# Optimization experiments

Measured on AMD Instinct MI355X. Metric: run time of the kernel, lower is better.

## Reference

```python
import jax, jax.numpy as jnp
import numpy as np
from jax import lax

NUM_HEADS = 8


def setup_inputs() -> dict:
    key = jax.random.key(0)
    ks = jax.random.split(key, 6)
    B, L, Hd = 4, 4096, 512
    S = 45  # factor * ceil(ln(L)) = 5 * 9
    x = jax.random.normal(ks[0], (B, L, Hd), dtype=jnp.float32)
    scale = 1.0 / np.sqrt(Hd)
    Wq = jax.random.normal(ks[1], (Hd, Hd), dtype=jnp.float32) * scale
    Wk = jax.random.normal(ks[2], (Hd, Hd), dtype=jnp.float32) * scale
    Wv = jax.random.normal(ks[3], (Hd, Hd), dtype=jnp.float32) * scale
    Wo = jax.random.normal(ks[4], (Hd, Hd), dtype=jnp.float32) * scale
    index_sample = jax.random.randint(ks[5], (L, S), 0, L, dtype=jnp.int32)
    return {"x": x, "Wq": Wq, "Wk": Wk, "Wv": Wv, "Wo": Wo,
            "index_sample": index_sample}


def reference(x, Wq, Wk, Wv, Wo, index_sample):
    B, L, Hd = x.shape
    H = NUM_HEADS
    D = Hd // H
    S = index_sample.shape[1]
    u = S  # n_top active queries = factor*ceil(ln(L))

    def split_heads(t):  # [B,L,Hd] -> [B,H,L,D]
        return t.reshape(B, L, H, D).transpose(0, 2, 1, 3)

    q = split_heads(x @ Wq)
    k = split_heads(x @ Wk)
    v = split_heads(x @ Wv)

    scale = 1.0 / jnp.sqrt(jnp.asarray(D, dtype=x.dtype))

    # sampled key gather: [B,H,L,S,D]
    K_samp = k[:, :, index_sample, :]
    # sampled scores per query: [B,H,L,S]
    QK_samp = jnp.einsum('bhld,bhlsd->bhls', q, K_samp)
    # sparsity measurement: max - mean over sampled keys
    M = QK_samp.max(axis=-1) - QK_samp.mean(axis=-1)  # [B,H,L]
    _, top_idx = lax.top_k(M, u)                      # [B,H,u]

    # full attention only for active queries
    Qr = jnp.take_along_axis(q, top_idx[..., None], axis=2)   # [B,H,u,D]
    scores = jnp.einsum('bhud,bhld->bhul', Qr, k) * scale     # [B,H,u,L]
    attn = jax.nn.softmax(scores, axis=-1)
    ctx_sel = jnp.einsum('bhul,bhld->bhud', attn, v)          # [B,H,u,D]

    # inactive queries get mean(V); scatter active results in
    context = jnp.broadcast_to(v.mean(axis=2, keepdims=True), (B, H, L, D))
    b_idx = jnp.arange(B)[:, None, None]
    h_idx = jnp.arange(H)[None, :, None]
    context = context.at[b_idx, h_idx, top_idx].set(ctx_sel)

    out = context.transpose(0, 2, 1, 3).reshape(B, L, Hd) @ Wo
    return out
```

## Files before the change

kernel.cpp:

```cpp
#include <hip/hip_runtime.h>
#include <cmath>

#define SS 45
#define FSPLIT 16

typedef __attribute__((ext_vector_type(8))) _Float16 half8;
typedef __attribute__((ext_vector_type(4))) float float4v;

__device__ inline unsigned short f16b(float f) {
    union { _Float16 h; unsigned short u; } c;
    c.h = (_Float16)f;
    return c.u;
}
__device__ inline float f16back(unsigned short u) {
    union { _Float16 h; unsigned short u; } c;
    c.u = u;
    return (float)c.h;
}

__device__ __forceinline__ void async16(const void* g, void* l) {
    __builtin_amdgcn_global_load_lds(
        (const __attribute__((address_space(1))) void*)g,
        (__attribute__((address_space(3))) void*)l, 16, 0, 0);
}

template <int CTRL>
__device__ __forceinline__ float dppadd(float v) {
    int x = __builtin_amdgcn_mov_dpp(__float_as_int(v), CTRL, 0xF, 0xF, true);
    return v + __int_as_float(x);
}
template <int CTRL>
__device__ __forceinline__ float dppmax(float v) {
    int x = __builtin_amdgcn_mov_dpp(__float_as_int(v), CTRL, 0xF, 0xF, true);
    return fmaxf(v, __int_as_float(x));
}

__global__ __launch_bounds__(256) void conv_kernel(
    const float4* __restrict__ x4, ushort4* __restrict__ xh4, ushort4* __restrict__ xl4,
    const float* __restrict__ Wq, const float* __restrict__ Wk, const float* __restrict__ Wv,
    unsigned short* __restrict__ WTh, unsigned short* __restrict__ WTl,
    float* __restrict__ vmp)
{
    int bid = blockIdx.x;
    if (bid < 8192) {
        int i = bid * 256 + threadIdx.x;
        float4 v = x4[i];
        float fv[4] = {v.x, v.y, v.z, v.w};
        ushort4 h, l;
        unsigned short hh[4], ll[4];
        #pragma unroll
        for (int e = 0; e < 4; e++) {
            hh[e] = f16b(fv[e]);
            ll[e] = f16b(fv[e] - f16back(hh[e]));
        }
        h.x = hh[0]; h.y = hh[1]; h.z = hh[2]; h.w = hh[3];
        l.x = ll[0]; l.y = ll[1]; l.z = ll[2]; l.w = ll[3];
        xh4[i] = h; xl4[i] = l;
    } else if (bid < 8960) {
        int wb = bid - 8192;
        int zy = wb >> 8;
        int bxy = wb & 255;
        const float* W = (zy == 0) ? Wq : (zy == 1) ? Wk : Wv;
        unsigned short* th = WTh + (size_t)zy * 262144;
        unsigned short* tl = WTl + (size_t)zy * 262144;
        __shared__ float t[32][33];
        int bx = bxy & 15, by = bxy >> 4;
        int tx = threadIdx.x & 31, ty = threadIdx.x >> 5;
        for (int i = ty; i < 32; i += 8) t[i][tx] = W[(size_t)(by * 32 + i) * 512 + bx * 32 + tx];
        __syncthreads();
        for (int i = ty; i < 32; i += 8) {
            float f = t[tx][i];
            unsigned short h = f16b(f);
            unsigned short lo = f16b(f - f16back(h));
            th[(size_t)(bx * 32 + i) * 512 + by * 32 + tx] = h;
            tl[(size_t)(bx * 32 + i) * 512 + by * 32 + tx] = lo;
        }
    } else {
        for (int i = threadIdx.x; i < 2048; i += 256) vmp[i] = 0.f;
    }
}

__global__ __launch_bounds__(512, 2) void qkv6_kernel(
    const unsigned short* __restrict__ Xh, const unsigned short* __restrict__ Xl,
    const unsigned short* __restrict__ WTh, const unsigned short* __restrict__ WTl,
    float* __restrict__ Q, float* __restrict__ K, float* __restrict__ V,
    float* __restrict__ vmp)
{
    __shared__ unsigned short lds[73728];

    int wave = threadIdx.x >> 6;
    int lane = threadIdx.x & 63;
    int m0blk = blockIdx.x * 256;
    int n0blk = blockIdx.y * 128;
    int fr = lane & 15;
    int C = lane >> 4;
    int srow = lane >> 2;
    int sslot = lane & 3;
    int mrb = (wave >> 1) * 64;
    int nrb = (wave & 1) * 64;

    const unsigned short* gb[7];
    gb[0] = Xh;
    gb[1] = Xl;
    gb[2] = WTh;
    gb[3] = WTl;
    gb[4] = WTh + 262144;
    gb[5] = WTl + 262144;
    gb[6] = WTh + 524288;

    float4v accq[4][4], acck[4][4], accv[4][4];
    #pragma unroll
    for (int i = 0; i < 4; i++)
        #pragma unroll
        for (int j = 0; j < 4; j++) {
            accq[i][j] = (float4v){0.f, 0.f, 0.f, 0.f};
            acck[i][j] = (float4v){0.f, 0.f, 0.f, 0.f};
            accv[i][j] = (float4v){0.f, 0.f, 0.f, 0.f};
        }

    auto stage = [&](int buf, int k0) {
        #pragma unroll
        for (int t = 0; t < 2; t++)
            #pragma unroll
            for (int inst = 0; inst < 2; inst++) {
                int rloc = wave * 32 + inst * 16 + srow;
                int Cp = sslot ^ ((rloc >> 1) & 3);
                const unsigned short* g = gb[t] + (size_t)(m0blk + rloc) * 512 + k0 + Cp * 8;
                async16(g, lds + buf * 36864 + t * 8192 + (wave * 32 + inst * 16) * 32);
            }
        #pragma unroll
        for (int t = 2; t < 7; t++) {
            int rloc = wave * 16 + srow;
            int Cp = sslot ^ ((rloc >> 1) & 3);
            const unsigned short* g = gb[t] + (size_t)(n0blk + rloc) * 512 + k0 + Cp * 8;
            async16(g, lds + buf * 36864 + 16384 + (t - 2) * 4096 + wave * 512);
        }
    };

    stage(0, 0);

    for (int kk = 0; kk < 16; kk++) {
        const unsigned short* Lb = lds + (kk & 1) * 36864;
        if (kk < 15) {
            stage((kk + 1) & 1, (kk + 1) * 32);
            asm volatile("s_waitcnt vmcnt(9)" ::: "memory");
        } else {
            asm volatile("s_waitcnt vmcnt(0)" ::: "memory");
        }
        __builtin_amdgcn_s_barrier();

        half8 A_h[4], A_l[4];
        #pragma unroll
        for (int i = 0; i < 4; i++) {
            int R = mrb + i * 16 + fr;
            int sl = C ^ ((R >> 1) & 3);
            A_h[i] = *(const half8*)(Lb + R * 32 + sl * 8);
            A_l[i] = *(const half8*)(Lb + 8192 + R * 32 + sl * 8);
        }
        #pragma unroll
        for (int j = 0; j < 4; j++) {
            int R = nrb + j * 16 + fr;
            int sl = C ^ ((R >> 1) & 3);
            int off = R * 32 + sl * 8;
            half8 Bqh = *(const half8*)(Lb + 16384 + off);
            half8 Bql = *(const half8*)(Lb + 20480 + off);
            half8 Bkh = *(const half8*)(Lb + 24576 + off);
            half8 Bkl = *(const half8*)(Lb + 28672 + off);
            half8 Bvh = *(const half8*)(Lb + 32768 + off);
            #pragma unroll
            for (int i = 0; i < 4; i++) {
                accq[i][j] = __builtin_amdgcn_mfma_f32_16x16x32_f16(A_h[i], Bqh, accq[i][j], 0, 0, 0);
                accq[i][j] = __builtin_amdgcn_mfma_f32_16x16x32_f16(A_h[i], Bql, accq[i][j], 0, 0, 0);
                accq[i][j] = __builtin_amdgcn_mfma_f32_16x16x32_f16(A_l[i], Bqh, accq[i][j], 0, 0, 0);
                acck[i][j] = __builtin_amdgcn_mfma_f32_16x16x32_f16(A_h[i], Bkh, acck[i][j], 0, 0, 0);
                acck[i][j] = __builtin_amdgcn_mfma_f32_16x16x32_f16(A_h[i], Bkl, acck[i][j], 0, 0, 0);
                acck[i][j] = __builtin_amdgcn_mfma_f32_16x16x32_f16(A_l[i], Bkh, acck[i][j], 0, 0, 0);
                accv[i][j] = __builtin_amdgcn_mfma_f32_16x16x32_f16(A_h[i], Bvh, accv[i][j], 0, 0, 0);
            }
        }
        __builtin_amdgcn_s_barrier();
    }

    int hh = n0blk + nrb;
    int hd = hh >> 6;
    int bb0 = (m0blk + mrb) >> 12;
    {
        float cs[4];
        #pragma unroll
        for (int j = 0; j < 4; j++) {
            float s = 0.f;
            #pragma unroll
            for (int i = 0; i < 4; i++)
                #pragma unroll
                for (int r = 0; r < 4; r++) s += accv[i][j][r];
            s += __shfl_xor(s, 16, 64);
            s += __shfl_xor(s, 32, 64);
            cs[j] = s;
        }
        if (C == 0) {
            #pragma unroll
            for (int j = 0; j < 4; j++)
                atomicAdd(vmp + ((size_t)(bb0 * 8 + hd) * 64) + j * 16 + fr, cs[j]);
        }
    }

    int rbase = C * 4;
    int m0 = m0blk + mrb;
    #pragma unroll
    for (int i = 0; i < 4; i++)
        #pragma unroll
        for (int r = 0; r < 4; r++) {
            int rg = m0 + i * 16 + rbase + r;
            int bb = rg >> 12, l = rg & 4095;
            size_t rowoff = ((size_t)(bb * 8 + hd) * 4096 + l) * 64;
            #pragma unroll
            for (int j = 0; j < 4; j++) Q[rowoff + j * 16 + fr] = accq[i][j][r];
            #pragma unroll
            for (int j = 0; j < 4; j++) K[rowoff + j * 16 + fr] = acck[i][j][r];
            #pragma unroll
            for (int j = 0; j < 4; j++) V[rowoff + j * 16 + fr] = accv[i][j][r];
        }
}

__global__ __launch_bounds__(256) void m_kernel(
    const float* __restrict__ Q, const float* __restrict__ K,
    const int* __restrict__ idx, float* __restrict__ M)
{
    int inst = blockIdx.x * 4 + (threadIdx.x >> 6);
    int lane = threadIdx.x & 63;
    int g = lane >> 3;
    int t = lane & 7;
    int bh = inst >> 12;
    int l = inst & 4095;
    float4 qa = *(const float4*)(Q + (size_t)inst * 64 + t * 4);
    float4 qb = *(const float4*)(Q + (size_t)inst * 64 + 32 + t * 4);
    const float* kb = K + (size_t)bh * 4096 * 64;
    const int* irow = idx + (size_t)l * SS;
    int jv[6];
    #pragma unroll
    for (int it = 0; it < 6; it++) {
        int s = it * 8 + g;
        jv[it] = irow[(it == 5 && g >= 5) ? 0 : s];
    }
    float4 kva[6], kvb[6];
    #pragma unroll
    for (int it = 0; it < 6; it++) {
        kva[it] = *(const float4*)(kb + (size_t)jv[it] * 64 + t * 4);
        kvb[it] = *(const float4*)(kb + (size_t)jv[it] * 64 + 32 + t * 4);
    }
    float maxv = -1e30f, sum = 0.f, p0 = 0.f;
    #pragma unroll
    for (int it = 0; it < 6; it++) {
        float p = qa.x * kva[it].x;
        p = fmaf(qa.y, kva[it].y, p);
        p = fmaf(qa.z, kva[it].z, p);
        p = fmaf(qa.w, kva[it].w, p);
        p = fmaf(qb.x, kvb[it].x, p);
        p = fmaf(qb.y, kvb[it].y, p);
        p = fmaf(qb.z, kvb[it].z, p);
        p = fmaf(qb.w, kvb[it].w, p);
        p = dppadd<0xB1>(p);
        p = dppadd<0x4E>(p);
        p = dppadd<0x141>(p);
        if (it == 0) p0 = p;
        maxv = fmaxf(maxv, p);
        sum += p;
    }
    maxv = dppmax<0x128>(maxv);
    maxv = fmaxf(maxv, __shfl_xor(maxv, 16, 64));
    maxv = fmaxf(maxv, __shfl_xor(maxv, 32, 64));
    sum = dppadd<0x128>(sum);
    sum += __shfl_xor(sum, 16, 64);
    sum += __shfl_xor(sum, 32, 64);
    float p0b = __shfl(p0, 0, 64);
    if (lane == 0) M[inst] = maxv - (sum - 3.f * p0b) * (1.f / 45.f);
}

__global__ __launch_bounds__(256) void topk_kernel(
    const float* __restrict__ M, int* __restrict__ tidx)
{
    int bh = blockIdx.x;
    __shared__ float vals[4096];
    __shared__ float wv[4];
    __shared__ int wi[4];
    int tid = threadIdx.x;
    int lane = tid & 63, w = tid >> 6;
    for (int i = tid; i < 4096; i += 256) vals[i] = M[(size_t)bh * 4096 + i];
    __syncthreads();
    for (int it = 0; it < SS; it++) {
        float bv = -1e38f; int bi = 0x7fffffff;
        for (int i = tid; i < 4096; i += 256) {
            float v = vals[i];
            if (v > bv) { bv = v; bi = i; }
        }
        #pragma unroll
        for (int s = 32; s > 0; s >>= 1) {
            float v2 = __shfl_xor(bv, s, 64);
            int i2 = __shfl_xor(bi, s, 64);
            if (v2 > bv || (v2 == bv && i2 < bi)) { bv = v2; bi = i2; }
        }
        if (lane == 0) { wv[w] = bv; wi[w] = bi; }
        __syncthreads();
        if (tid == 0) {
            float b0 = wv[0]; int i0 = wi[0];
            #pragma unroll
            for (int k = 1; k < 4; k++)
                if (wv[k] > b0 || (wv[k] == b0 && wi[k] < i0)) { b0 = wv[k]; i0 = wi[k]; }
            tidx[bh * SS + it] = i0;
            vals[i0] = -1e38f;
        }
        __syncthreads();
    }
}

__global__ __launch_bounds__(256) void base_kernel(
    const float* __restrict__ vmp, const float* __restrict__ Wo,
    float* __restrict__ vmean, float* __restrict__ base)
{
    int b = blockIdx.x;
    __shared__ float vmS[512];
    int tid = threadIdx.x;
    for (int i = tid; i < 512; i += 256) {
        float s = vmp[(size_t)b * 512 + i] * (1.f / 4096.f);
        vmS[i] = s;
        vmean[(size_t)b * 512 + i] = s;
    }
    __syncthreads();
    for (int j = tid; j < 512; j += 256) {
        float s = 0.f;
        for (int i = 0; i < 512; i++) s += vmS[i] * Wo[(size_t)i * 512 + j];
        base[(size_t)b * 512 + j] = s;
    }
}

__global__ __launch_bounds__(256) void attn_flash_kernel(
    const float* __restrict__ Q, const float* __restrict__ K, const float* __restrict__ V,
    const int* __restrict__ tidx,
    float* __restrict__ Opart, float* __restrict__ mpart, float* __restrict__ lpart)
{
    int split = blockIdx.x;
    int bh = blockIdx.y;
    int L0 = split * (4096 / FSPLIT);

    __shared__ float Qs[48][68];
    __shared__ float Ks[64][68];
    __shared__ float Vs[64][68];
    __shared__ float Ps[48][68];
    __shared__ int tS[48];

    int tid = threadIdx.x;
    int lane = tid & 63, w = tid >> 6;
    if (tid < 48) tS[tid] = (tid < SS) ? tidx[bh * SS + tid] : 0;
    __syncthreads();
    for (int u = w; u < 48; u += 4)
        Qs[u][lane] = Q[((size_t)bh * 4096 + tS[u]) * 64 + lane];

    int ug = tid >> 4, lg = tid & 15;
    float mrun[4], lrun[4], O[4][4];
    #pragma unroll
    for (int i = 0; i < 4; i++) {
        mrun[i] = -1e30f; lrun[i] = 0.f;
        #pragma unroll
        for (int j = 0; j < 4; j++) O[i][j] = 0.f;
    }

    for (int tt = 0; tt < 4096 / FSPLIT / 64; tt++) {
        int lbase = L0 + tt * 64;
        if (tt > 0) __syncthreads();
        for (int r = w; r < 64; r += 4) {
            Ks[r][lane] = K[((size_t)bh * 4096 + lbase + r) * 64 + lane];
            Vs[r][lane] = V[((size_t)bh * 4096 + lbase + r) * 64 + lane];
        }
        __syncthreads();

        if (tid < 192) {
            float acc[4][4];
            #pragma unroll
            for (int i = 0; i < 4; i++)
                #pragma unroll
                for (int j = 0; j < 4; j++) acc[i][j] = 0.f;
            for (int d0 = 0; d0 < 64; d0 += 4) {
                float4 a[4], b[4];
                #pragma unroll
                for (int i = 0; i < 4; i++) a[i] = *(float4*)&Qs[ug * 4 + i][d0];
                #pragma unroll
                for (int j = 0; j < 4; j++) b[j] = *(float4*)&Ks[lg * 4 + j][d0];
                #pragma unroll
                for (int i = 0; i < 4; i++)
                    #pragma unroll
                    for (int j = 0; j < 4; j++)
                        acc[i][j] += a[i].x * b[j].x + a[i].y * b[j].y + a[i].z * b[j].z + a[i].w * b[j].w;
            }
            #pragma unroll
            for (int i = 0; i < 4; i++) {
                #pragma unroll
                for (int j = 0; j < 4; j++) acc[i][j] *= 0.125f;
                float tm = fmaxf(fmaxf(acc[i][0], acc[i][1]), fmaxf(acc[i][2], acc[i][3]));
                tm = fmaxf(tm, __shfl_xor(tm, 1, 64));
                tm = fmaxf(tm, __shfl_xor(tm, 2, 64));
                tm = fmaxf(tm, __shfl_xor(tm, 4, 64));
                tm = fmaxf(tm, __shfl_xor(tm, 8, 64));
                float nm = fmaxf(mrun[i], tm);
                float corr = __expf(mrun[i] - nm);
                float rs = 0.f;
                #pragma unroll
                for (int j = 0; j < 4; j++) {
                    float p = __expf(acc[i][j] - nm);
                    Ps[ug * 4 + i][lg * 4 + j] = p;
                    rs += p;
                }
                rs += __shfl_xor(rs, 1, 64);
                rs += __shfl_xor(rs, 2, 64);
                rs += __shfl_xor(rs, 4, 64);
                rs += __shfl_xor(rs, 8, 64);
                lrun[i] = lrun[i] * corr + rs;
                mrun[i] = nm;
                #pragma unroll
                for (int j = 0; j < 4; j++) O[i][j] *= corr;
            }
        }
        __syncthreads();

        if (tid < 192) {
            for (int l0 = 0; l0 < 64; l0 += 4) {
                float4 vr[4];
                #pragma unroll
                for (int r = 0; r < 4; r++) vr[r] = *(float4*)&Vs[l0 + r][lg * 4];
                #pragma unroll
                for (int i = 0; i < 4; i++) {
                    float4 pv = *(float4*)&Ps[ug * 4 + i][l0];
                    #pragma unroll
                    for (int j = 0; j < 4; j++) {
                        float vj0 = (&vr[0].x)[j], vj1 = (&vr[1].x)[j];
                        float vj2 = (&vr[2].x)[j], vj3 = (&vr[3].x)[j];
                        O[i][j] = fmaf(pv.x, vj0, fmaf(pv.y, vj1, fmaf(pv.z, vj2, fmaf(pv.w, vj3, O[i][j]))));
                    }
                }
            }
        }
    }

    if (tid < 192) {
        #pragma unroll
        for (int i = 0; i < 4; i++) {
            int u = ug * 4 + i;
            if (u < SS) {
                size_t pbase = ((size_t)(bh * FSPLIT + split) * SS + u);
                if (lg == 0) { mpart[pbase] = mrun[i]; lpart[pbase] = lrun[i]; }
                #pragma unroll
                for (int j = 0; j < 4; j++)
                    Opart[pbase * 64 + lg * 4 + j] = O[i][j];
            }
        }
    }
}

__global__ __launch_bounds__(256) void combine_kernel(
    const float* __restrict__ Opart, const float* __restrict__ mpart, const float* __restrict__ lpart,
    const float* __restrict__ vmean, const float* __restrict__ Wo,
    const int* __restrict__ tidx, float* __restrict__ out)
{
    int rr = blockIdx.x;
    int bh = rr / SS, u = rr % SS;
    int h = bh & 7, b = bh >> 3;
    __shared__ float dS[64];
    int tid = threadIdx.x;
    if (tid < 64) {
        float m = -1e30f;
        #pragma unroll
        for (int s = 0; s < FSPLIT; s++)
            m = fmaxf(m, mpart[(size_t)(bh * FSPLIT + s) * SS + u]);
        float den = 0.f, num = 0.f;
        #pragma unroll
        for (int s = 0; s < FSPLIT; s++) {
            size_t pbase = (size_t)(bh * FSPLIT + s) * SS + u;
            float wgt = __expf(mpart[pbase] - m);
            den += wgt * lpart[pbase];
            num += wgt * Opart[pbase * 64 + tid];
        }
        dS[tid] = num / den - vmean[(size_t)bh * 64 + tid];
    }
    __syncthreads();
    int l = tidx[rr];
    float* orow = out + ((size_t)b * 4096 + l) * 512;
    for (int j = tid; j < 512; j += 256) {
        float s = 0.f;
        #pragma unroll
        for (int dd = 0; dd < 64; dd++) s += dS[dd] * Wo[(size_t)(h * 64 + dd) * 512 + j];
        atomicAdd(orow + j, s);
    }
}

__global__ __launch_bounds__(256) void fill_kernel(
    const float4* __restrict__ base4, float4* __restrict__ out4)
{
    int i = blockIdx.x * 256 + threadIdx.x;
    int b = i >> 19;
    int j4 = i & 127;
    out4[i] = base4[b * 128 + j4];
}

extern "C" void kernel_launch(void* const* d_in, const int* in_sizes, int n_in,
                              void* d_out, int out_size, void* d_ws, size_t ws_size,
                              hipStream_t stream)
{
    const float* x  = (const float*)d_in[0];
    const float* Wq = (const float*)d_in[1];
    const float* Wk = (const float*)d_in[2];
    const float* Wv = (const float*)d_in[3];
    const float* Wo = (const float*)d_in[4];
    const int*  idx = (const int*)d_in[5];
    float* out = (float*)d_out;

    float* W = (float*)d_ws;
    float* Q = W;
    float* K = W + 8388608;
    float* V = W + 16777216;
    unsigned short* xh  = (unsigned short*)(W + 25165824);
    unsigned short* xl  = (unsigned short*)(W + 29360128);
    unsigned short* WTh = (unsigned short*)(W + 33554432);
    unsigned short* WTl = (unsigned short*)(W + 33947648);
    float* vmp = W + 34340864;

    float* Mv    = W + 25165824;
    float* Opart = W + 25296896;
    float* mpart = W + 26771456;
    float* lpart = W + 26794496;
    float* vmean = W + 33439744;
    float* base  = W + 33441792;
    int*   tidx  = (int*)(W + 33443840);

    conv_kernel<<<8961, 256, 0, stream>>>((const float4*)x, (ushort4*)xh, (ushort4*)xl,
                                          Wq, Wk, Wv, WTh, WTl, vmp);
    qkv6_kernel<<<dim3(64, 4), 512, 0, stream>>>(xh, xl, WTh, WTl, Q, K, V, vmp);
    m_kernel<<<32768, 256, 0, stream>>>(Q, K, idx, Mv);
    topk_kernel<<<32, 256, 0, stream>>>(Mv, tidx);
    base_kernel<<<4, 256, 0, stream>>>(vmp, Wo, vmean, base);
    fill_kernel<<<8192, 256, 0, stream>>>((const float4*)base, (float4*)out);
    attn_flash_kernel<<<dim3(FSPLIT, 32), 256, 0, stream>>>(Q, K, V, tidx, Opart, mpart, lpart);
    combine_kernel<<<1440, 256, 0, stream>>>(Opart, mpart, lpart, vmean, Wo, tidx, out);
}
```

Measured before the change: 474.3 us.

## Replace serial top-k with two-stage bitonic sort and fuse small kernels

Replaces the serial 45-iteration argmax top-k, which ran on only 32 blocks, with a two-stage selection. In the first stage, 256 blocks bitonic-sort 512-element chunks of sortable 64-bit keys (monotone float bits plus a reversed index) and keep the top 45 of each chunk. In the second stage, 32 blocks merge those candidates by sorting again. The base/mean computation is folded into the merge launch, and the fill of the output is folded into the attention launch, which cuts the launch count. The tie-break by lowest index is kept through the reversed index in the key.

```diff
diff --git a/kernel.cpp b/kernel.cpp
--- a/kernel.cpp
+++ b/kernel.cpp
@@ -33,6 +33,11 @@
 __device__ __forceinline__ float dppmax(float v) {
     int x = __builtin_amdgcn_mov_dpp(__float_as_int(v), CTRL, 0xF, 0xF, true);
     return fmaxf(v, __int_as_float(x));
+}
+
+__device__ __forceinline__ unsigned int fmono(float f) {
+    unsigned int u = __float_as_uint(f);
+    return (u & 0x80000000u) ? ~u : (u | 0x80000000u);
 }
 
 __global__ __launch_bounds__(256) void conv_kernel(
@@ -276,70 +281,98 @@
     if (lane == 0) M[inst] = maxv - (sum - 3.f * p0b) * (1.f / 45.f);
 }
 
-__global__ __launch_bounds__(256) void topk_kernel(
-    const float* __restrict__ M, int* __restrict__ tidx)
-{
-    int bh = blockIdx.x;
-    __shared__ float vals[4096];
-    __shared__ float wv[4];
-    __shared__ int wi[4];
+__global__ __launch_bounds__(256) void topk_local_kernel(
+    const float* __restrict__ M, unsigned long long* __restrict__ cand)
+{
+    int chunk = blockIdx.x;
+    int bh = chunk >> 3, c = chunk & 7;
+    __shared__ unsigned long long keys[512];
     int tid = threadIdx.x;
-    int lane = tid & 63, w = tid >> 6;
-    for (int i = tid; i < 4096; i += 256) vals[i] = M[(size_t)bh * 4096 + i];
+    for (int i = tid; i < 512; i += 256) {
+        int l = c * 512 + i;
+        unsigned int u = fmono(M[(size_t)bh * 4096 + l]);
+        keys[i] = ((unsigned long long)u << 32) | (unsigned int)(4095 - l);
+    }
     __syncthreads();
-    for (int it = 0; it < SS; it++) {
-        float bv = -1e38f; int bi = 0x7fffffff;
-        for (int i = tid; i < 4096; i += 256) {
-            float v = vals[i];
-            if (v > bv) { bv = v; bi = i; }
-        }
-        #pragma unroll
-        for (int s = 32; s > 0; s >>= 1) {
-            float v2 = __shfl_xor(bv, s, 64);
-            int i2 = __shfl_xor(bi, s, 64);
-            if (v2 > bv || (v2 == bv && i2 < bi)) { bv = v2; bi = i2; }
-        }
-        if (lane == 0) { wv[w] = bv; wi[w] = bi; }
-        __syncthreads();
-        if (tid == 0) {
-            float b0 = wv[0]; int i0 = wi[0];
-            #pragma unroll
-            for (int k = 1; k < 4; k++)
-                if (wv[k] > b0 || (wv[k] == b0 && wi[k] < i0)) { b0 = wv[k]; i0 = wi[k]; }
-            tidx[bh * SS + it] = i0;
-            vals[i0] = -1e38f;
-        }
-        __syncthreads();
-    }
-}
-
-__global__ __launch_bounds__(256) void base_kernel(
+    for (int k = 2; k <= 512; k <<= 1)
+        for (int j = k >> 1; j > 0; j >>= 1) {
+            for (int i0 = tid; i0 < 512; i0 += 256) {
+                int ixj = i0 ^ j;
+                if (ixj > i0) {
+                    unsigned long long a = keys[i0], b = keys[ixj];
+                    bool asc = (i0 & k) != 0;
+                    if (asc ? (a > b) : (a < b)) { keys[i0] = b; keys[ixj] = a; }
+                }
+            }
+            __syncthreads();
+        }
+    if (tid < SS) cand[(size_t)chunk * SS + tid] = keys[tid];
+}
+
+__global__ __launch_bounds__(256) void topk_merge_base_kernel(
+    const unsigned long long* __restrict__ cand, int* __restrict__ tidx,
     const float* __restrict__ vmp, const float* __restrict__ Wo,
     float* __restrict__ vmean, float* __restrict__ base)
 {
-    int b = blockIdx.x;
-    __shared__ float vmS[512];
+    int bid = blockIdx.x;
     int tid = threadIdx.x;
-    for (int i = tid; i < 512; i += 256) {
-        float s = vmp[(size_t)b * 512 + i] * (1.f / 4096.f);
-        vmS[i] = s;
-        vmean[(size_t)b * 512 + i] = s;
-    }
-    __syncthreads();
-    for (int j = tid; j < 512; j += 256) {
-        float s = 0.f;
-        for (int i = 0; i < 512; i++) s += vmS[i] * Wo[(size_t)i * 512 + j];
-        base[(size_t)b * 512 + j] = s;
-    }
-}
-
-__global__ __launch_bounds__(256) void attn_flash_kernel(
+    if (bid < 32) {
+        __shared__ unsigned long long keys[512];
+        for (int i = tid; i < 512; i += 256) {
+            unsigned long long v = 0ull;
+            if (i < 8 * SS) {
+                int cc = i / SS, r = i - cc * SS;
+                v = cand[((size_t)bid * 8 + cc) * SS + r];
+            }
+            keys[i] = v;
+        }
+        __syncthreads();
+        for (int k = 2; k <= 512; k <<= 1)
+            for (int j = k >> 1; j > 0; j >>= 1) {
+                for (int i0 = tid; i0 < 512; i0 += 256) {
+                    int ixj = i0 ^ j;
+                    if (ixj > i0) {
+                        unsigned long long a = keys[i0], b = keys[ixj];
+                        bool asc = (i0 & k) != 0;
+                        if (asc ? (a > b) : (a < b)) { keys[i0] = b; keys[ixj] = a; }
+                    }
+                }
+                __syncthreads();
+            }
+        if (tid < SS) tidx[bid * SS + tid] = 4095 - (int)(keys[tid] & 0xFFFFFFFFu);
+    } else {
+        int b = bid - 32;
+        __shared__ float vmS[512];
+        for (int i = tid; i < 512; i += 256) {
+            float s = vmp[(size_t)b * 512 + i] * (1.f / 4096.f);
+            vmS[i] = s;
+            vmean[(size_t)b * 512 + i] = s;
+        }
+        __syncthreads();
+        for (int jj = tid; jj < 512; jj += 256) {
+            float s = 0.f;
+            for (int i = 0; i < 512; i++) s += vmS[i] * Wo[(size_t)i * 512 + jj];
+            base[(size_t)b * 512 + jj] = s;
+        }
+    }
+}
+
+__global__ __launch_bounds__(256) void attn_fill_kernel(
     const float* __restrict__ Q, const float* __restrict__ K, const float* __restrict__ V,
     const int* __restrict__ tidx,
-    float* __restrict__ Opart, float* __restrict__ mpart, float* __restrict__ lpart)
-{
-    int split = blockIdx.x;
-    int bh = blockIdx.y;
+    float* __restrict__ Opart, float* __restrict__ mpart, float* __restrict__ lpart,
+    const float4* __restrict__ base4, float4* __restrict__ out4)
+{
+    int bid = blockIdx.x;
+    if (bid >= 512) {
+        int i = (bid - 512) * 256 + threadIdx.x;
+        int b = i >> 19;
+        int j4 = i & 127;
+        out4[i] = base4[b * 128 + j4];
+        return;
+    }
+    int split = bid & 15;
+    int bh = bid >> 4;
     int L0 = split * (4096 / FSPLIT);
 
     __shared__ float Qs[48][68];
@@ -491,15 +524,6 @@
     }
 }
 
-__global__ __launch_bounds__(256) void fill_kernel(
-    const float4* __restrict__ base4, float4* __restrict__ out4)
-{
-    int i = blockIdx.x * 256 + threadIdx.x;
-    int b = i >> 19;
-    int j4 = i & 127;
-    out4[i] = base4[b * 128 + j4];
-}
-
 extern "C" void kernel_launch(void* const* d_in, const int* in_sizes, int n_in,
                               void* d_out, int out_size, void* d_ws, size_t ws_size,
                               hipStream_t stream)
@@ -529,14 +553,15 @@
     float* vmean = W + 33439744;
     float* base  = W + 33441792;
     int*   tidx  = (int*)(W + 33443840);
+    unsigned long long* cand = (unsigned long long*)(W + 33445280);
 
     conv_kernel<<<8961, 256, 0, stream>>>((const float4*)x, (ushort4*)xh, (ushort4*)xl,
                                           Wq, Wk, Wv, WTh, WTl, vmp);
     qkv6_kernel<<<dim3(64, 4), 512, 0, stream>>>(xh, xl, WTh, WTl, Q, K, V, vmp);
     m_kernel<<<32768, 256, 0, stream>>>(Q, K, idx, Mv);
-    topk_kernel<<<32, 256, 0, stream>>>(Mv, tidx);
-    base_kernel<<<4, 256, 0, stream>>>(vmp, Wo, vmean, base);
-    fill_kernel<<<8192, 256, 0, stream>>>((const float4*)base, (float4*)out);
-    attn_flash_kernel<<<dim3(FSPLIT, 32), 256, 0, stream>>>(Q, K, V, tidx, Opart, mpart, lpart);
+    topk_local_kernel<<<256, 256, 0, stream>>>(Mv, cand);
+    topk_merge_base_kernel<<<36, 256, 0, stream>>>(cand, tidx, vmp, Wo, vmean, base);
+    attn_fill_kernel<<<512 + 8192, 256, 0, stream>>>(Q, K, V, tidx, Opart, mpart, lpart,
+                                                     (const float4*)base, (float4*)out);
     combine_kernel<<<1440, 256, 0, stream>>>(Opart, mpart, lpart, vmean, Wo, tidx, out);
 }
```

Result: faster. 408.8 us (-13.8%).
